# Performance work log

Hardware: AMD Instinct MI355X
Metric: run time of the kernel (lower is better)

## Reference

```python
import jax, jax.numpy as jnp
import numpy as np

N, D, K, H = 262144, 128, 10, 128  # batch, input_dim, num_bins, hidden width


def mlp(x, w1, b1, w2, b2, w3, b3):
    h = jax.nn.relu(x @ w1 + b1)
    h = jax.nn.relu(h @ w2 + b2)
    return h @ w3 + b3


def rq_spline(x, widths, heights, derivatives):
    # x: [N, D]; widths/heights: [N, K]; derivatives: [N, K+1]
    x = jnp.clip(x, 1e-5, 1.0 - 1e-5)
    bin_widths = jax.nn.softmax(widths, axis=-1)
    bin_heights = jax.nn.softmax(heights, axis=-1)
    bin_derivs = jax.nn.softplus(derivatives)
    cum_w = jnp.pad(jnp.cumsum(bin_widths, axis=-1), ((0, 0), (1, 0)))  # [N, K+1], starts at 0
    # data-dependent bin search: count knots strictly below each element
    bin_idx = jnp.sum(x[..., None] > cum_w[:, None, :], axis=-1) - 1  # [N, D] in [0, K-1]
    row = jnp.arange(x.shape[0])[:, None]  # [N, 1] for per-row gathers
    left = cum_w[row, bin_idx]            # [N, D]
    right = cum_w[row, bin_idx + 1]       # [N, D]
    w = jnp.maximum(right - left, 1e-5)
    theta = (x - left) / w
    h_k = bin_heights[row, bin_idx]
    h_k1 = bin_heights[row, bin_idx + 1]   # jax clamps the out-of-range last index
    d_k = bin_derivs[row, bin_idx]
    d_k1 = bin_derivs[row, bin_idx + 1]
    one_m = 1.0 - theta
    numerator = h_k * theta * theta + d_k * theta * one_m
    denominator = h_k1 * one_m * one_m + d_k1 * theta * one_m
    return left + w * numerator / denominator


def setup_inputs() -> dict:
    key = jax.random.key(0)
    ks = jax.random.split(key, 19)
    s = 1.0 / np.sqrt(H)
    x = jax.random.uniform(ks[0], (N, D), dtype=jnp.float32)

    def lin(k, din, dout):
        kw, kb = jax.random.split(k)
        return (jax.random.normal(kw, (din, dout), jnp.float32) * s,
                jax.random.normal(kb, (dout,), jnp.float32) * s)

    ww1, wb1 = lin(ks[1], D, H)
    ww2, wb2 = lin(ks[2], H, H)
    ww3, wb3 = lin(ks[3], H, K)
    hw1, hb1 = lin(ks[4], D, H)
    hw2, hb2 = lin(ks[5], H, H)
    hw3, hb3 = lin(ks[6], H, K)
    dw1, db1 = lin(ks[7], D, H)
    dw2, db2 = lin(ks[8], H, H)
    dw3, db3 = lin(ks[9], H, K + 1)
    return dict(x=x, ww1=ww1, wb1=wb1, ww2=ww2, wb2=wb2, ww3=ww3, wb3=wb3,
                hw1=hw1, hb1=hb1, hw2=hw2, hb2=hb2, hw3=hw3, hb3=hb3,
                dw1=dw1, db1=db1, dw2=dw2, db2=db2, dw3=dw3, db3=db3)


def reference(x, ww1, wb1, ww2, wb2, ww3, wb3,
              hw1, hb1, hw2, hb2, hw3, hb3,
              dw1, db1, dw2, db2, dw3, db3):
    widths = mlp(x, ww1, wb1, ww2, wb2, ww3, wb3)          # [N, K]
    heights = mlp(x, hw1, hb1, hw2, hb2, hw3, hb3)          # [N, K]
    derivatives = mlp(x, dw1, db1, dw2, db2, dw3, db3)      # [N, K+1]
    return rq_spline(x, widths, heights, derivatives)
```

## Files before the change

### kernel.cpp

```cpp
#include <hip/hip_runtime.h>
#include <hip/hip_bf16.h>
#include <math.h>

#define TPB 256
#define RB  128
#define HPB 136

typedef __attribute__((ext_vector_type(8))) short bf16x8;
typedef __attribute__((ext_vector_type(4))) float f32x4;

#define MLP_LDS 68656


__device__ __forceinline__ short f2bf(float f) {
    union { __hip_bfloat16 b; short s; } cv;
    cv.b = __float2bfloat16(f);
    return cv.s;
}

__device__ __forceinline__ void gload16(const void* g, void* l) {
    __builtin_amdgcn_global_load_lds(
        (const __attribute__((address_space(1))) void*)g,
        (__attribute__((address_space(3))) void*)l, 16, 0, 0);
}

__device__ __forceinline__ void stageW(const ushort* g, ushort* l, int iters, int wave, int lane) {
    const char* gs = (const char*)g + wave * iters * 1024;
    char* ls = (char*)l + wave * iters * 1024;
    for (int i = 0; i < iters; ++i)
        gload16(gs + i * 1024 + lane * 16, ls + i * 1024 + lane * 16);
}

__global__ void prep_kernel(const float* __restrict__ ww1, const float* __restrict__ ww2, const float* __restrict__ ww3,
                            const float* __restrict__ hw1, const float* __restrict__ hw2, const float* __restrict__ hw3,
                            const float* __restrict__ dw1, const float* __restrict__ dw2, const float* __restrict__ dw3,
                            ushort* __restrict__ ws) {
    int bid = blockIdx.x;
    int k = threadIdx.x;
    const float* W; int KK, base, n;
    if      (bid < 128) { W = ww1; KK = 128; base = 0;      n = bid; }
    else if (bid < 256) { W = ww2; KK = 128; base = 16384;  n = bid - 128; }
    else if (bid < 272) { W = ww3; KK = 10;  base = 32768;  n = bid - 256; }
    else if (bid < 400) { W = hw1; KK = 128; base = 34816;  n = bid - 272; }
    else if (bid < 528) { W = hw2; KK = 128; base = 51200;  n = bid - 400; }
    else if (bid < 544) { W = hw3; KK = 10;  base = 67584;  n = bid - 528; }
    else if (bid < 672) { W = dw1; KK = 128; base = 69632;  n = bid - 544; }
    else if (bid < 800) { W = dw2; KK = 128; base = 86016;  n = bid - 672; }
    else                { W = dw3; KK = 11;  base = 102400; n = bid - 800; }
    float v = (n < KK) ? W[k * KK + n] : 0.0f;
    int chunk = (k >> 3) ^ (n & 7);
    ws[base + n * 128 + chunk * 8 + (k & 7)] = (ushort)f2bf(v);
}

__device__ __forceinline__ void big_layer(ushort* XH, const ushort* Wt, const float* biasL,
                                          int bofs, int wave, int lane) {
    const int m = lane & 15, g = lane >> 4;
    bf16x8 af[2][4];
    #pragma unroll
    for (int mt = 0; mt < 2; ++mt) {
        const ushort* ar = XH + ((wave << 5) + (mt << 4) + m) * HPB + (g << 3);
        #pragma unroll
        for (int q = 0; q < 4; ++q)
            af[mt][q] = *(const bf16x8*)(ar + (q << 5));
    }
    f32x4 acc[2][8];
    #pragma unroll
    for (int mt = 0; mt < 2; ++mt)
        #pragma unroll
        for (int nt = 0; nt < 8; ++nt) acc[mt][nt] = (f32x4){0.f, 0.f, 0.f, 0.f};
    #pragma unroll
    for (int nt = 0; nt < 8; ++nt) {
        const int n = (nt << 4) + m;
        const ushort* bp = Wt + n * 128;
        bf16x8 bf[4];
        #pragma unroll
        for (int q = 0; q < 4; ++q)
            bf[q] = *(const bf16x8*)(bp + ((((q << 2) + g) ^ (n & 7)) << 3));
        #pragma unroll
        for (int mt = 0; mt < 2; ++mt)
            #pragma unroll
            for (int q = 0; q < 4; ++q)
                acc[mt][nt] = __builtin_amdgcn_mfma_f32_16x16x32_bf16(af[mt][q], bf[q], acc[mt][nt], 0, 0, 0);
    }
    #pragma unroll
    for (int mt = 0; mt < 2; ++mt) {
        const int orow = (wave << 5) + (mt << 4) + (g << 2);
        #pragma unroll
        for (int nt = 0; nt < 8; ++nt) {
            float bb = biasL[bofs + (nt << 4) + m];
            #pragma unroll
            for (int r = 0; r < 4; ++r)
                XH[(orow + r) * HPB + (nt << 4) + m] = (ushort)f2bf(fmaxf(acc[mt][nt][r] + bb, 0.f));
        }
    }
}

__device__ __forceinline__ void small_layer(const ushort* XH, const ushort* Wt, const float* biasL,
                                            int KK, int my, float* outp, int wave, int lane) {
    const int m = lane & 15, g = lane >> 4;
    bf16x8 af[2][4];
    #pragma unroll
    for (int mt = 0; mt < 2; ++mt) {
        const ushort* ar = XH + ((wave << 5) + (mt << 4) + m) * HPB + (g << 3);
        #pragma unroll
        for (int q = 0; q < 4; ++q)
            af[mt][q] = *(const bf16x8*)(ar + (q << 5));
    }
    bf16x8 bf[4];
    const ushort* bp = Wt + m * 128;
    #pragma unroll
    for (int q = 0; q < 4; ++q)
        bf[q] = *(const bf16x8*)(bp + ((((q << 2) + g) ^ (m & 7)) << 3));
    f32x4 acc[2];
    acc[0] = (f32x4){0.f, 0.f, 0.f, 0.f};
    acc[1] = (f32x4){0.f, 0.f, 0.f, 0.f};
    #pragma unroll
    for (int mt = 0; mt < 2; ++mt)
        #pragma unroll
        for (int q = 0; q < 4; ++q)
            acc[mt] = __builtin_amdgcn_mfma_f32_16x16x32_bf16(af[mt][q], bf[q], acc[mt], 0, 0, 0);
    if (m < KK) {
        float bb = biasL[256 + m];
        #pragma unroll
        for (int mt = 0; mt < 2; ++mt) {
            const int orow = (wave << 5) + (mt << 4) + (g << 2);
            #pragma unroll
            for (int r = 0; r < 4; ++r)
                outp[(long long)(orow + r) * 128 + my * 12 + m] = acc[mt][r] + bb;
        }
    }
}

__global__ __launch_bounds__(TPB, 2) void mlp_kernel(
    const float* __restrict__ x,
    const float* __restrict__ wb1, const float* __restrict__ wb2, const float* __restrict__ wb3,
    const float* __restrict__ hb1, const float* __restrict__ hb2, const float* __restrict__ hb3,
    const float* __restrict__ db1, const float* __restrict__ db2, const float* __restrict__ db3,
    const ushort* __restrict__ wsb,
    float* __restrict__ out) {
    extern __shared__ char smem[];
    ushort* XH    = (ushort*)smem;
    ushort* Wt    = (ushort*)(smem + 34816);
    float*  biasL = (float*)(smem + 67584);

    const int t = threadIdx.x;
    const int wave = t >> 6, lane = t & 63;
    const int my = blockIdx.y;
    const long long row0 = (long long)blockIdx.x * RB;

    const float *B1, *B2, *B3;
    if (my == 0)      { B1 = wb1; B2 = wb2; B3 = wb3; }
    else if (my == 1) { B1 = hb1; B2 = hb2; B3 = hb3; }
    else              { B1 = db1; B2 = db2; B3 = db3; }
    const ushort* W = wsb + my * 34816;
    const int KK3 = (my == 2) ? 11 : 10;

    stageW(W, Wt, 8, wave, lane);

    {
        const float4* xg = (const float4*)(x + row0 * 128);
        #pragma unroll
        for (int i = 0; i < 8; ++i) {
            int idx = i * TPB + t;
            int r = idx >> 4, c8 = idx & 15;
            float4 u = xg[idx * 2];
            float4 v = xg[idx * 2 + 1];
            bf16x8 a;
            a[0] = f2bf(u.x); a[1] = f2bf(u.y); a[2] = f2bf(u.z); a[3] = f2bf(u.w);
            a[4] = f2bf(v.x); a[5] = f2bf(v.y); a[6] = f2bf(v.z); a[7] = f2bf(v.w);
            *(bf16x8*)(XH + r * HPB + c8 * 8) = a;
        }
    }
    if (t < 128) { biasL[t] = B1[t]; biasL[128 + t] = B2[t]; }
    else { int u = t - 128; if (u < KK3) biasL[256 + u] = B3[u]; }
    __syncthreads();

    big_layer(XH, Wt, biasL, 0, wave, lane);
    __syncthreads();
    stageW(W + 16384, Wt, 8, wave, lane);
    __syncthreads();
    big_layer(XH, Wt, biasL, 128, wave, lane);
    __syncthreads();
    stageW(W + 32768, Wt, 1, wave, lane);
    __syncthreads();
    small_layer(XH, Wt, biasL, KK3, my, out + row0 * 128, wave, lane);
}

__global__ void spline_kernel(const float* __restrict__ x, float* __restrict__ out) {
    __shared__ float obase[3 * 64 * 12];
    float* ow = obase;
    float* oh = obase + 768;
    float* od = obase + 1536;
    const int t = threadIdx.x;
    const long long row0 = (long long)blockIdx.x * 64;

    for (int j = t; j < 64 * 36; j += TPB) {
        int r = j / 36, c = j % 36;
        float v = out[(row0 + r) * 128 + c];
        int wh = c / 12, cc = c % 12;
        obase[wh * 768 + r * 12 + cc] = v;
    }
    __syncthreads();

    if (t < 192) {
        int r = t & 63;
        int which = t >> 6;
        if (which == 0) {
            float v[10];
            #pragma unroll
            for (int j = 0; j < 10; ++j) v[j] = ow[r * 12 + j];
            float mx = v[0];
            #pragma unroll
            for (int j = 1; j < 10; ++j) mx = fmaxf(mx, v[j]);
            float e[10], s = 0.f;
            #pragma unroll
            for (int j = 0; j < 10; ++j) { e[j] = expf(v[j] - mx); s += e[j]; }
            float c = 0.f;
            ow[r * 12 + 0] = 0.f;
            #pragma unroll
            for (int j = 0; j < 10; ++j) { c += e[j] / s; ow[r * 12 + j + 1] = c; }
        } else if (which == 1) {
            float v[10];
            #pragma unroll
            for (int j = 0; j < 10; ++j) v[j] = oh[r * 12 + j];
            float mx = v[0];
            #pragma unroll
            for (int j = 1; j < 10; ++j) mx = fmaxf(mx, v[j]);
            float e[10], s = 0.f;
            #pragma unroll
            for (int j = 0; j < 10; ++j) { e[j] = expf(v[j] - mx); s += e[j]; }
            float last = 0.f;
            #pragma unroll
            for (int j = 0; j < 10; ++j) { last = e[j] / s; oh[r * 12 + j] = last; }
            oh[r * 12 + 10] = last;
        } else {
            #pragma unroll
            for (int j = 0; j < 11; ++j) {
                float v = od[r * 12 + j];
                od[r * 12 + j] = fmaxf(v, 0.f) + log1pf(expf(-fabsf(v)));
            }
        }
    }
    __syncthreads();

    for (int idx = t; idx < 64 * 128; idx += TPB) {
        int r = idx >> 7;
        float xv = x[row0 * 128 + idx];
        xv = fminf(fmaxf(xv, 1e-5f), 1.0f - 1e-5f);
        const float* cw = ow + r * 12;
        int bin = -1;
        #pragma unroll
        for (int j = 0; j < 11; ++j) bin += (xv > cw[j]) ? 1 : 0;
        bin = max(0, min(bin, 9));
        float left = cw[bin], right = cw[bin + 1];
        float w = fmaxf(right - left, 1e-5f);
        float th = (xv - left) / w;
        float om = 1.0f - th;
        float hk  = oh[r * 12 + bin], hk1 = oh[r * 12 + bin + 1];
        float dk  = od[r * 12 + bin], dk1 = od[r * 12 + bin + 1];
        float num = hk * th * th + dk * th * om;
        float den = hk1 * om * om + dk1 * th * om;
        float res = left + w * num / den;
        res = (fabsf(res) < 3.0e38f) ? res : 0.0f;
        out[row0 * 128 + idx] = res;
    }
}

extern "C" void kernel_launch(void* const* d_in, const int* in_sizes, int n_in,
                              void* d_out, int out_size, void* d_ws, size_t ws_size,
                              hipStream_t stream) {
    const float* x   = (const float*)d_in[0];
    const float* ww1 = (const float*)d_in[1];
    const float* wb1 = (const float*)d_in[2];
    const float* ww2 = (const float*)d_in[3];
    const float* wb2 = (const float*)d_in[4];
    const float* ww3 = (const float*)d_in[5];
    const float* wb3 = (const float*)d_in[6];
    const float* hw1 = (const float*)d_in[7];
    const float* hb1 = (const float*)d_in[8];
    const float* hw2 = (const float*)d_in[9];
    const float* hb2 = (const float*)d_in[10];
    const float* hw3 = (const float*)d_in[11];
    const float* hb3 = (const float*)d_in[12];
    const float* dw1 = (const float*)d_in[13];
    const float* db1 = (const float*)d_in[14];
    const float* dw2 = (const float*)d_in[15];
    const float* db2 = (const float*)d_in[16];
    const float* dw3 = (const float*)d_in[17];
    const float* db3 = (const float*)d_in[18];
    float* out = (float*)d_out;
    ushort* ws = (ushort*)d_ws;

    const int N = in_sizes[0] / 128;
    const int nb_mlp = N / RB;
    const int nb_spl = N / 64;

    prep_kernel<<<dim3(816), dim3(128), 0, stream>>>(ww1, ww2, ww3, hw1, hw2, hw3,
                                                     dw1, dw2, dw3, ws);

    (void)hipFuncSetAttribute((const void*)mlp_kernel,
                              hipFuncAttributeMaxDynamicSharedMemorySize, MLP_LDS);

    mlp_kernel<<<dim3(nb_mlp, 3), dim3(TPB), MLP_LDS, stream>>>(
        x, wb1, wb2, wb3, hb1, hb2, hb3, db1, db2, db3, ws, out);

    spline_kernel<<<dim3(nb_spl), dim3(TPB), 0, stream>>>(x, out);
}
```

Measured before the change: 416.5 us.

## Prefetch layer-2/3 weights into registers and interleave MLP heads per row tile

The layer-2 and layer-3 weights are now loaded into registers at kernel start, so their global latency overlaps the x load and the first layer. After layer 1 they are written to LDS, with a separate LDS region for the layer-3 weights, which removes two barriers and a staging round-trip. The grid is flattened so the three MLP heads for the same row tile run as adjacent blocks and can share x in cache. The x load is made wave-local, and the spline's x reads and output writes are vectorized to float4. In exchange there is more register pressure (36 extra VGPRs per thread) and a slightly larger LDS footprint, which may reduce occupancy.

Result: slower. 461.1 us (+10.7%).

```diff
diff --git a/kernel.cpp b/kernel.cpp
--- a/kernel.cpp
+++ b/kernel.cpp
@@ -9,7 +9,7 @@
 typedef __attribute__((ext_vector_type(8))) short bf16x8;
 typedef __attribute__((ext_vector_type(4))) float f32x4;
 
-#define MLP_LDS 68656
+#define MLP_LDS 72752
 
 
 __device__ __forceinline__ short f2bf(float f) {
@@ -95,7 +95,7 @@
     }
 }
 
-__device__ __forceinline__ void small_layer(const ushort* XH, const ushort* Wt, const float* biasL,
+__device__ __forceinline__ void small_layer(const ushort* XH, const ushort* W3s, const float* biasL,
                                             int KK, int my, float* outp, int wave, int lane) {
     const int m = lane & 15, g = lane >> 4;
     bf16x8 af[2][4];
@@ -107,7 +107,7 @@
             af[mt][q] = *(const bf16x8*)(ar + (q << 5));
     }
     bf16x8 bf[4];
-    const ushort* bp = Wt + m * 128;
+    const ushort* bp = W3s + m * 128;
     #pragma unroll
     for (int q = 0; q < 4; ++q)
         bf[q] = *(const bf16x8*)(bp + ((((q << 2) + g) ^ (m & 7)) << 3));
@@ -141,12 +141,14 @@
     extern __shared__ char smem[];
     ushort* XH    = (ushort*)smem;
     ushort* Wt    = (ushort*)(smem + 34816);
-    float*  biasL = (float*)(smem + 67584);
+    ushort* W3s   = (ushort*)(smem + 67584);
+    float*  biasL = (float*)(smem + 71680);
 
     const int t = threadIdx.x;
     const int wave = t >> 6, lane = t & 63;
-    const int my = blockIdx.y;
-    const long long row0 = (long long)blockIdx.x * RB;
+    const int bid = blockIdx.x;
+    const int my = bid % 3;
+    const long long row0 = (long long)(bid / 3) * RB;
 
     const float *B1, *B2, *B3;
     if (my == 0)      { B1 = wb1; B2 = wb2; B3 = wb3; }
@@ -156,19 +158,26 @@
     const int KK3 = (my == 2) ? 11 : 10;
 
     stageW(W, Wt, 8, wave, lane);
-
+    uint4 w2r[8];
     {
-        const float4* xg = (const float4*)(x + row0 * 128);
+        const char* w2g = (const char*)(W + 16384) + wave * 8192 + lane * 16;
+        #pragma unroll
+        for (int i = 0; i < 8; ++i) w2r[i] = *(const uint4*)(w2g + i * 1024);
+    }
+    uint4 w3r = *(const uint4*)((const char*)(W + 32768) + wave * 1024 + lane * 16);
+
+    {
+        const float* xg = x + (row0 + (wave << 5)) * 128;
         #pragma unroll
         for (int i = 0; i < 8; ++i) {
-            int idx = i * TPB + t;
-            int r = idx >> 4, c8 = idx & 15;
-            float4 u = xg[idx * 2];
-            float4 v = xg[idx * 2 + 1];
+            int flat = i * 64 + lane;
+            int r = flat >> 4, c8 = flat & 15;
+            float4 u = *(const float4*)(xg + r * 128 + c8 * 8);
+            float4 v = *(const float4*)(xg + r * 128 + c8 * 8 + 4);
             bf16x8 a;
             a[0] = f2bf(u.x); a[1] = f2bf(u.y); a[2] = f2bf(u.z); a[3] = f2bf(u.w);
             a[4] = f2bf(v.x); a[5] = f2bf(v.y); a[6] = f2bf(v.z); a[7] = f2bf(v.w);
-            *(bf16x8*)(XH + r * HPB + c8 * 8) = a;
+            *(bf16x8*)(XH + ((wave << 5) + r) * HPB + c8 * 8) = a;
         }
     }
     if (t < 128) { biasL[t] = B1[t]; biasL[128 + t] = B2[t]; }
@@ -177,13 +186,15 @@
 
     big_layer(XH, Wt, biasL, 0, wave, lane);
     __syncthreads();
-    stageW(W + 16384, Wt, 8, wave, lane);
+    {
+        char* w2l = (char*)Wt + wave * 8192 + lane * 16;
+        #pragma unroll
+        for (int i = 0; i < 8; ++i) *(uint4*)(w2l + i * 1024) = w2r[i];
+        *(uint4*)((char*)W3s + wave * 1024 + lane * 16) = w3r;
+    }
     __syncthreads();
     big_layer(XH, Wt, biasL, 128, wave, lane);
-    __syncthreads();
-    stageW(W + 32768, Wt, 1, wave, lane);
-    __syncthreads();
-    small_layer(XH, Wt, biasL, KK3, my, out + row0 * 128, wave, lane);
+    small_layer(XH, W3s, biasL, KK3, my, out + row0 * 128, wave, lane);
 }
 
 __global__ void spline_kernel(const float* __restrict__ x, float* __restrict__ out) {
@@ -243,26 +254,31 @@
     }
     __syncthreads();
 
-    for (int idx = t; idx < 64 * 128; idx += TPB) {
-        int r = idx >> 7;
-        float xv = x[row0 * 128 + idx];
-        xv = fminf(fmaxf(xv, 1e-5f), 1.0f - 1e-5f);
+    for (int it = t; it < 64 * 32; it += TPB) {
+        int r = it >> 5, c4 = it & 31;
         const float* cw = ow + r * 12;
-        int bin = -1;
-        #pragma unroll
-        for (int j = 0; j < 11; ++j) bin += (xv > cw[j]) ? 1 : 0;
-        bin = max(0, min(bin, 9));
-        float left = cw[bin], right = cw[bin + 1];
-        float w = fmaxf(right - left, 1e-5f);
-        float th = (xv - left) / w;
-        float om = 1.0f - th;
-        float hk  = oh[r * 12 + bin], hk1 = oh[r * 12 + bin + 1];
-        float dk  = od[r * 12 + bin], dk1 = od[r * 12 + bin + 1];
-        float num = hk * th * th + dk * th * om;
-        float den = hk1 * om * om + dk1 * th * om;
-        float res = left + w * num / den;
-        res = (fabsf(res) < 3.0e38f) ? res : 0.0f;
-        out[row0 * 128 + idx] = res;
+        float4 xv4 = *(const float4*)(x + (row0 + r) * 128 + c4 * 4);
+        float rf[4];
+        float xin[4] = {xv4.x, xv4.y, xv4.z, xv4.w};
+        #pragma unroll
+        for (int e = 0; e < 4; ++e) {
+            float xv = fminf(fmaxf(xin[e], 1e-5f), 1.0f - 1e-5f);
+            int bin = -1;
+            #pragma unroll
+            for (int j = 0; j < 11; ++j) bin += (xv > cw[j]) ? 1 : 0;
+            bin = max(0, min(bin, 9));
+            float left = cw[bin], right = cw[bin + 1];
+            float w = fmaxf(right - left, 1e-5f);
+            float th = (xv - left) / w;
+            float om = 1.0f - th;
+            float hk  = oh[r * 12 + bin], hk1 = oh[r * 12 + bin + 1];
+            float dk  = od[r * 12 + bin], dk1 = od[r * 12 + bin + 1];
+            float num = hk * th * th + dk * th * om;
+            float den = hk1 * om * om + dk1 * th * om;
+            float res = left + w * num / den;
+            rf[e] = (fabsf(res) < 3.0e38f) ? res : 0.0f;
+        }
+        *(float4*)(out + (row0 + r) * 128 + c4 * 4) = make_float4(rf[0], rf[1], rf[2], rf[3]);
     }
 }
 
@@ -292,7 +308,7 @@
     ushort* ws = (ushort*)d_ws;
 
     const int N = in_sizes[0] / 128;
-    const int nb_mlp = N / RB;
+    const int nb_mlp = (N / RB) * 3;
     const int nb_spl = N / 64;
 
     prep_kernel<<<dim3(816), dim3(128), 0, stream>>>(ww1, ww2, ww3, hw1, hw2, hw3,
@@ -301,7 +317,7 @@
     (void)hipFuncSetAttribute((const void*)mlp_kernel,
                               hipFuncAttributeMaxDynamicSharedMemorySize, MLP_LDS);
 
-    mlp_kernel<<<dim3(nb_mlp, 3), dim3(TPB), MLP_LDS, stream>>>(
+    mlp_kernel<<<dim3(nb_mlp), dim3(TPB), MLP_LDS, stream>>>(
         x, wb1, wb2, wb3, hb1, hb2, hb3, db1, db2, db3, ws, out);
 
     spline_kernel<<<dim3(nb_spl), dim3(TPB), 0, stream>>>(x, out);
```

## Read MLP weights directly from global/L2 instead of staging them into LDS

Applied to the files above, without the earlier changes.

The MLP kernel no longer stages each layer's bf16 weights into shared memory. MFMA B-fragments are now loaded directly from global memory, which should stay in L2/cache because the weights are small. The first-layer A-fragments are built straight from global x, so most block-wide barriers disappear. LDS drops to the activation tile only, which allows four blocks per CU instead of two. The spline stage is also vectorised to float4 loads and stores, at the cost of more global traffic per wave for weight reads.

After: 527.9 us. +26.8%, slower.

```diff
diff --git a/kernel.cpp b/kernel.cpp
--- a/kernel.cpp
+++ b/kernel.cpp
@@ -8,27 +8,12 @@
 
 typedef __attribute__((ext_vector_type(8))) short bf16x8;
 typedef __attribute__((ext_vector_type(4))) float f32x4;
-
-#define MLP_LDS 68656
 
 
 __device__ __forceinline__ short f2bf(float f) {
     union { __hip_bfloat16 b; short s; } cv;
     cv.b = __float2bfloat16(f);
     return cv.s;
-}
-
-__device__ __forceinline__ void gload16(const void* g, void* l) {
-    __builtin_amdgcn_global_load_lds(
-        (const __attribute__((address_space(1))) void*)g,
-        (__attribute__((address_space(3))) void*)l, 16, 0, 0);
-}
-
-__device__ __forceinline__ void stageW(const ushort* g, ushort* l, int iters, int wave, int lane) {
-    const char* gs = (const char*)g + wave * iters * 1024;
-    char* ls = (char*)l + wave * iters * 1024;
-    for (int i = 0; i < iters; ++i)
-        gload16(gs + i * 1024 + lane * 16, ls + i * 1024 + lane * 16);
 }
 
 __global__ void prep_kernel(const float* __restrict__ ww1, const float* __restrict__ ww2, const float* __restrict__ ww3,
@@ -48,14 +33,46 @@
     else if (bid < 800) { W = dw2; KK = 128; base = 86016;  n = bid - 672; }
     else                { W = dw3; KK = 11;  base = 102400; n = bid - 800; }
     float v = (n < KK) ? W[k * KK + n] : 0.0f;
-    int chunk = (k >> 3) ^ (n & 7);
-    ws[base + n * 128 + chunk * 8 + (k & 7)] = (ushort)f2bf(v);
-}
-
-__device__ __forceinline__ void big_layer(ushort* XH, const ushort* Wt, const float* biasL,
-                                          int bofs, int wave, int lane) {
-    const int m = lane & 15, g = lane >> 4;
-    bf16x8 af[2][4];
+    ws[base + n * 128 + k] = (ushort)f2bf(v);
+}
+
+__device__ __forceinline__ void big_compute(const bf16x8 af[2][4], const ushort* __restrict__ Wg,
+                                            const float* __restrict__ bg, ushort* XH,
+                                            int wave, int m, int g) {
+    f32x4 acc[2][8];
+    #pragma unroll
+    for (int mt = 0; mt < 2; ++mt)
+        #pragma unroll
+        for (int nt = 0; nt < 8; ++nt) acc[mt][nt] = (f32x4){0.f, 0.f, 0.f, 0.f};
+    #pragma unroll
+    for (int nt = 0; nt < 8; ++nt) {
+        const ushort* bp = Wg + (((nt << 4) + m) << 7) + (g << 3);
+        bf16x8 b0 = *(const bf16x8*)(bp);
+        bf16x8 b1 = *(const bf16x8*)(bp + 32);
+        bf16x8 b2 = *(const bf16x8*)(bp + 64);
+        bf16x8 b3 = *(const bf16x8*)(bp + 96);
+        #pragma unroll
+        for (int mt = 0; mt < 2; ++mt) {
+            acc[mt][nt] = __builtin_amdgcn_mfma_f32_16x16x32_bf16(af[mt][0], b0, acc[mt][nt], 0, 0, 0);
+            acc[mt][nt] = __builtin_amdgcn_mfma_f32_16x16x32_bf16(af[mt][1], b1, acc[mt][nt], 0, 0, 0);
+            acc[mt][nt] = __builtin_amdgcn_mfma_f32_16x16x32_bf16(af[mt][2], b2, acc[mt][nt], 0, 0, 0);
+            acc[mt][nt] = __builtin_amdgcn_mfma_f32_16x16x32_bf16(af[mt][3], b3, acc[mt][nt], 0, 0, 0);
+        }
+    }
+    #pragma unroll
+    for (int nt = 0; nt < 8; ++nt) {
+        float bb = bg[(nt << 4) + m];
+        #pragma unroll
+        for (int mt = 0; mt < 2; ++mt) {
+            const int orow = (wave << 5) + (mt << 4) + (g << 2);
+            #pragma unroll
+            for (int r = 0; r < 4; ++r)
+                XH[(orow + r) * HPB + (nt << 4) + m] = (ushort)f2bf(fmaxf(acc[mt][nt][r] + bb, 0.f));
+        }
+    }
+}
+
+__device__ __forceinline__ void load_af_lds(const ushort* XH, bf16x8 af[2][4], int wave, int m, int g) {
     #pragma unroll
     for (int mt = 0; mt < 2; ++mt) {
         const ushort* ar = XH + ((wave << 5) + (mt << 4) + m) * HPB + (g << 3);
@@ -63,88 +80,20 @@
         for (int q = 0; q < 4; ++q)
             af[mt][q] = *(const bf16x8*)(ar + (q << 5));
     }
-    f32x4 acc[2][8];
-    #pragma unroll
-    for (int mt = 0; mt < 2; ++mt)
-        #pragma unroll
-        for (int nt = 0; nt < 8; ++nt) acc[mt][nt] = (f32x4){0.f, 0.f, 0.f, 0.f};
-    #pragma unroll
-    for (int nt = 0; nt < 8; ++nt) {
-        const int n = (nt << 4) + m;
-        const ushort* bp = Wt + n * 128;
-        bf16x8 bf[4];
-        #pragma unroll
-        for (int q = 0; q < 4; ++q)
-            bf[q] = *(const bf16x8*)(bp + ((((q << 2) + g) ^ (n & 7)) << 3));
-        #pragma unroll
-        for (int mt = 0; mt < 2; ++mt)
-            #pragma unroll
-            for (int q = 0; q < 4; ++q)
-                acc[mt][nt] = __builtin_amdgcn_mfma_f32_16x16x32_bf16(af[mt][q], bf[q], acc[mt][nt], 0, 0, 0);
-    }
-    #pragma unroll
-    for (int mt = 0; mt < 2; ++mt) {
-        const int orow = (wave << 5) + (mt << 4) + (g << 2);
-        #pragma unroll
-        for (int nt = 0; nt < 8; ++nt) {
-            float bb = biasL[bofs + (nt << 4) + m];
-            #pragma unroll
-            for (int r = 0; r < 4; ++r)
-                XH[(orow + r) * HPB + (nt << 4) + m] = (ushort)f2bf(fmaxf(acc[mt][nt][r] + bb, 0.f));
-        }
-    }
-}
-
-__device__ __forceinline__ void small_layer(const ushort* XH, const ushort* Wt, const float* biasL,
-                                            int KK, int my, float* outp, int wave, int lane) {
-    const int m = lane & 15, g = lane >> 4;
-    bf16x8 af[2][4];
-    #pragma unroll
-    for (int mt = 0; mt < 2; ++mt) {
-        const ushort* ar = XH + ((wave << 5) + (mt << 4) + m) * HPB + (g << 3);
-        #pragma unroll
-        for (int q = 0; q < 4; ++q)
-            af[mt][q] = *(const bf16x8*)(ar + (q << 5));
-    }
-    bf16x8 bf[4];
-    const ushort* bp = Wt + m * 128;
-    #pragma unroll
-    for (int q = 0; q < 4; ++q)
-        bf[q] = *(const bf16x8*)(bp + ((((q << 2) + g) ^ (m & 7)) << 3));
-    f32x4 acc[2];
-    acc[0] = (f32x4){0.f, 0.f, 0.f, 0.f};
-    acc[1] = (f32x4){0.f, 0.f, 0.f, 0.f};
-    #pragma unroll
-    for (int mt = 0; mt < 2; ++mt)
-        #pragma unroll
-        for (int q = 0; q < 4; ++q)
-            acc[mt] = __builtin_amdgcn_mfma_f32_16x16x32_bf16(af[mt][q], bf[q], acc[mt], 0, 0, 0);
-    if (m < KK) {
-        float bb = biasL[256 + m];
-        #pragma unroll
-        for (int mt = 0; mt < 2; ++mt) {
-            const int orow = (wave << 5) + (mt << 4) + (g << 2);
-            #pragma unroll
-            for (int r = 0; r < 4; ++r)
-                outp[(long long)(orow + r) * 128 + my * 12 + m] = acc[mt][r] + bb;
-        }
-    }
-}
-
-__global__ __launch_bounds__(TPB, 2) void mlp_kernel(
+}
+
+__global__ __launch_bounds__(TPB, 4) void mlp_kernel(
     const float* __restrict__ x,
     const float* __restrict__ wb1, const float* __restrict__ wb2, const float* __restrict__ wb3,
     const float* __restrict__ hb1, const float* __restrict__ hb2, const float* __restrict__ hb3,
     const float* __restrict__ db1, const float* __restrict__ db2, const float* __restrict__ db3,
     const ushort* __restrict__ wsb,
     float* __restrict__ out) {
-    extern __shared__ char smem[];
-    ushort* XH    = (ushort*)smem;
-    ushort* Wt    = (ushort*)(smem + 34816);
-    float*  biasL = (float*)(smem + 67584);
+    __shared__ ushort XH[RB * HPB];
 
     const int t = threadIdx.x;
     const int wave = t >> 6, lane = t & 63;
+    const int m = lane & 15, g = lane >> 4;
     const int my = blockIdx.y;
     const long long row0 = (long long)blockIdx.x * RB;
 
@@ -155,35 +104,53 @@
     const ushort* W = wsb + my * 34816;
     const int KK3 = (my == 2) ? 11 : 10;
 
-    stageW(W, Wt, 8, wave, lane);
-
-    {
-        const float4* xg = (const float4*)(x + row0 * 128);
-        #pragma unroll
-        for (int i = 0; i < 8; ++i) {
-            int idx = i * TPB + t;
-            int r = idx >> 4, c8 = idx & 15;
-            float4 u = xg[idx * 2];
-            float4 v = xg[idx * 2 + 1];
+    bf16x8 af[2][4];
+    #pragma unroll
+    for (int mt = 0; mt < 2; ++mt) {
+        const float* xr = x + (row0 + (wave << 5) + (mt << 4) + m) * 128 + (g << 3);
+        #pragma unroll
+        for (int q = 0; q < 4; ++q) {
+            float4 u = *(const float4*)(xr + (q << 5));
+            float4 v = *(const float4*)(xr + (q << 5) + 4);
             bf16x8 a;
             a[0] = f2bf(u.x); a[1] = f2bf(u.y); a[2] = f2bf(u.z); a[3] = f2bf(u.w);
             a[4] = f2bf(v.x); a[5] = f2bf(v.y); a[6] = f2bf(v.z); a[7] = f2bf(v.w);
-            *(bf16x8*)(XH + r * HPB + c8 * 8) = a;
-        }
-    }
-    if (t < 128) { biasL[t] = B1[t]; biasL[128 + t] = B2[t]; }
-    else { int u = t - 128; if (u < KK3) biasL[256 + u] = B3[u]; }
-    __syncthreads();
-
-    big_layer(XH, Wt, biasL, 0, wave, lane);
-    __syncthreads();
-    stageW(W + 16384, Wt, 8, wave, lane);
-    __syncthreads();
-    big_layer(XH, Wt, biasL, 128, wave, lane);
-    __syncthreads();
-    stageW(W + 32768, Wt, 1, wave, lane);
-    __syncthreads();
-    small_layer(XH, Wt, biasL, KK3, my, out + row0 * 128, wave, lane);
+            af[mt][q] = a;
+        }
+    }
+    big_compute(af, W, B1, XH, wave, m, g);
+
+    load_af_lds(XH, af, wave, m, g);
+    big_compute(af, W + 16384, B2, XH, wave, m, g);
+
+    load_af_lds(XH, af, wave, m, g);
+    {
+        const ushort* bp = W + 32768 + (m << 7) + (g << 3);
+        bf16x8 b0 = *(const bf16x8*)(bp);
+        bf16x8 b1 = *(const bf16x8*)(bp + 32);
+        bf16x8 b2 = *(const bf16x8*)(bp + 64);
+        bf16x8 b3 = *(const bf16x8*)(bp + 96);
+        f32x4 acc[2];
+        acc[0] = (f32x4){0.f, 0.f, 0.f, 0.f};
+        acc[1] = (f32x4){0.f, 0.f, 0.f, 0.f};
+        #pragma unroll
+        for (int mt = 0; mt < 2; ++mt) {
+            acc[mt] = __builtin_amdgcn_mfma_f32_16x16x32_bf16(af[mt][0], b0, acc[mt], 0, 0, 0);
+            acc[mt] = __builtin_amdgcn_mfma_f32_16x16x32_bf16(af[mt][1], b1, acc[mt], 0, 0, 0);
+            acc[mt] = __builtin_amdgcn_mfma_f32_16x16x32_bf16(af[mt][2], b2, acc[mt], 0, 0, 0);
+            acc[mt] = __builtin_amdgcn_mfma_f32_16x16x32_bf16(af[mt][3], b3, acc[mt], 0, 0, 0);
+        }
+        if (m < KK3) {
+            float bb = B3[m];
+            #pragma unroll
+            for (int mt = 0; mt < 2; ++mt) {
+                const int orow = (wave << 5) + (mt << 4) + (g << 2);
+                #pragma unroll
+                for (int r = 0; r < 4; ++r)
+                    out[(row0 + orow + r) * 128 + my * 12 + m] = acc[mt][r] + bb;
+            }
+        }
+    }
 }
 
 __global__ void spline_kernel(const float* __restrict__ x, float* __restrict__ out) {
@@ -243,26 +210,31 @@
     }
     __syncthreads();
 
-    for (int idx = t; idx < 64 * 128; idx += TPB) {
-        int r = idx >> 7;
-        float xv = x[row0 * 128 + idx];
-        xv = fminf(fmaxf(xv, 1e-5f), 1.0f - 1e-5f);
+    for (int it = t; it < 64 * 32; it += TPB) {
+        int r = it >> 5, c4 = it & 31;
         const float* cw = ow + r * 12;
-        int bin = -1;
-        #pragma unroll
-        for (int j = 0; j < 11; ++j) bin += (xv > cw[j]) ? 1 : 0;
-        bin = max(0, min(bin, 9));
-        float left = cw[bin], right = cw[bin + 1];
-        float w = fmaxf(right - left, 1e-5f);
-        float th = (xv - left) / w;
-        float om = 1.0f - th;
-        float hk  = oh[r * 12 + bin], hk1 = oh[r * 12 + bin + 1];
-        float dk  = od[r * 12 + bin], dk1 = od[r * 12 + bin + 1];
-        float num = hk * th * th + dk * th * om;
-        float den = hk1 * om * om + dk1 * th * om;
-        float res = left + w * num / den;
-        res = (fabsf(res) < 3.0e38f) ? res : 0.0f;
-        out[row0 * 128 + idx] = res;
+        float4 xv4 = *(const float4*)(x + (row0 + r) * 128 + c4 * 4);
+        float rf[4];
+        float xin[4] = {xv4.x, xv4.y, xv4.z, xv4.w};
+        #pragma unroll
+        for (int e = 0; e < 4; ++e) {
+            float xv = fminf(fmaxf(xin[e], 1e-5f), 1.0f - 1e-5f);
+            int bin = -1;
+            #pragma unroll
+            for (int j = 0; j < 11; ++j) bin += (xv > cw[j]) ? 1 : 0;
+            bin = max(0, min(bin, 9));
+            float left = cw[bin], right = cw[bin + 1];
+            float w = fmaxf(right - left, 1e-5f);
+            float th = (xv - left) / w;
+            float om = 1.0f - th;
+            float hk  = oh[r * 12 + bin], hk1 = oh[r * 12 + bin + 1];
+            float dk  = od[r * 12 + bin], dk1 = od[r * 12 + bin + 1];
+            float num = hk * th * th + dk * th * om;
+            float den = hk1 * om * om + dk1 * th * om;
+            float res = left + w * num / den;
+            rf[e] = (fabsf(res) < 3.0e38f) ? res : 0.0f;
+        }
+        *(float4*)(out + (row0 + r) * 128 + c4 * 4) = make_float4(rf[0], rf[1], rf[2], rf[3]);
     }
 }
 
@@ -298,10 +270,7 @@
     prep_kernel<<<dim3(816), dim3(128), 0, stream>>>(ww1, ww2, ww3, hw1, hw2, hw3,
                                                      dw1, dw2, dw3, ws);
 
-    (void)hipFuncSetAttribute((const void*)mlp_kernel,
-                              hipFuncAttributeMaxDynamicSharedMemorySize, MLP_LDS);
-
-    mlp_kernel<<<dim3(nb_mlp, 3), dim3(TPB), MLP_LDS, stream>>>(
+    mlp_kernel<<<dim3(nb_mlp, 3), dim3(TPB), 0, stream>>>(
         x, wb1, wb2, wb3, hb1, hb2, hb3, db1, db2, db3, ws, out);
 
     spline_kernel<<<dim3(nb_spl), dim3(TPB), 0, stream>>>(x, out);
```
